# Kernel tuning notes

Hardware: AMD Instinct MI355X
Metric: run time of the kernel (lower is better)

Reference implementation:

```python
import jax, jax.numpy as jnp
import numpy as np

# bucket boundaries from the original module; bucket = last index with width >= bin
BUCKET_BINS = jnp.array([0, 1, 2, 3, 4, 5, 7, 8, 15, 16, 31, 32, 63, 64], dtype=jnp.int32)


def setup_inputs() -> dict:
    key = jax.random.key(0)
    k1, k2, k3, k4, k5 = jax.random.split(key, 5)
    B, S, D, E = 16, 512, 768, 128   # batch, n_spans, span_dim, distance_embeddings_dim
    T, O = 64, 64                    # targets / opinions per batch element
    spans = jax.random.normal(k1, (B, S, D), dtype=jnp.float32)
    dist_emb = jax.random.normal(k2, (len(BUCKET_BINS), E), dtype=jnp.float32) * 0.02
    span_indices = jnp.sort(jax.random.randint(k3, (S, 2), 0, 128, dtype=jnp.int32), axis=1)
    target_indices = jax.random.randint(k4, (B, T), 0, S, dtype=jnp.int32)
    opinion_indices = jax.random.randint(k5, (B, O), 0, S, dtype=jnp.int32)
    return {"spans": spans, "dist_emb": dist_emb, "span_indices": span_indices,
            "target_indices": target_indices, "opinion_indices": opinion_indices}


def reference(spans, dist_emb, span_indices, target_indices, opinion_indices):
    # spans: [B,S,D]; span_indices: [S,2]; target/opinion_indices: [B,T]/[B,O]
    B, T = target_indices.shape
    O = opinion_indices.shape[1]
    # itertools.product order: for each target, iterate all opinions
    pair_t = jnp.repeat(target_indices, O, axis=1)      # [B, P] with P = T*O
    pair_o = jnp.tile(opinion_indices, (1, T))          # [B, P]
    # gather span representations
    span_t = jnp.take_along_axis(spans, pair_t[:, :, None], axis=1)  # [B,P,D]
    span_o = jnp.take_along_axis(spans, pair_o[:, :, None], axis=1)  # [B,P,D]
    # gather (a,b) / (c,d) word positions and compute min distance
    ab = span_indices[pair_t]                            # [B,P,2]
    cd = span_indices[pair_o]                            # [B,P,2]
    a, b = ab[..., 0], ab[..., 1]
    c, d = cd[..., 0], cd[..., 1]
    width = jnp.minimum(jnp.abs(b - c), jnp.abs(a - d))  # [B,P]
    # bucketize: last index with width >= BUCKET_BINS[idx]
    bucket = jnp.searchsorted(BUCKET_BINS, width.astype(jnp.int32), side="right") - 1
    dist = dist_emb[bucket]                              # [B,P,E]
    # G(St, So) = [St; So; f_distance]
    out = jnp.concatenate([span_t, span_o, dist], axis=-1)  # [B,P,2D+E]
    return out
```

## Files before the change

kernel.cpp:

```cpp
#include <hip/hip_runtime.h>


#define B_DIM 16
#define S_DIM 512
#define D_DIM 768
#define E_DIM 128
#define T_DIM 64
#define O_DIM 64
#define ROW_FLOATS (2 * D_DIM + E_DIM)
#define ROW_F4 (ROW_FLOATS / 4)
#define D_F4 (D_DIM / 4)

typedef float f32x4 __attribute__((ext_vector_type(4)));

__global__ __launch_bounds__(256) void pair_rep_kernel(
    const float* __restrict__ spans,
    const float* __restrict__ dist_emb,
    const int*   __restrict__ span_indices,
    const int*   __restrict__ target_indices,
    const int*   __restrict__ opinion_indices,
    float*       __restrict__ out)
{
    const int row = blockIdx.x;
    const int b   = row >> 12;
    const int p   = row & 4095;
    const int t   = p >> 6;
    const int o   = p & 63;

    const int ti = target_indices[b * T_DIM + t];
    const int oi = opinion_indices[b * O_DIM + o];

    const int a_ = span_indices[2 * ti];
    const int b_ = span_indices[2 * ti + 1];
    const int c_ = span_indices[2 * oi];
    const int d_ = span_indices[2 * oi + 1];
    const int w1 = abs(b_ - c_);
    const int w2 = abs(a_ - d_);
    const int width = min(w1, w2);

    const int bins[14] = {0, 1, 2, 3, 4, 5, 7, 8, 15, 16, 31, 32, 63, 64};
    int bucket = -1;
#pragma unroll
    for (int i = 0; i < 14; ++i) bucket += (width >= bins[i]) ? 1 : 0;

    const f32x4* st = (const f32x4*)(spans + ((size_t)b * S_DIM + ti) * D_DIM);
    const f32x4* so = (const f32x4*)(spans + ((size_t)b * S_DIM + oi) * D_DIM);
    const f32x4* de = (const f32x4*)(dist_emb + (size_t)bucket * E_DIM);
    f32x4* dst = (f32x4*)(out + (size_t)row * ROW_FLOATS);

    for (int c4 = threadIdx.x; c4 < ROW_F4; c4 += 256) {
        f32x4 v;
        if (c4 < D_F4) {
            v = st[c4];
        } else if (c4 < 2 * D_F4) {
            v = so[c4 - D_F4];
        } else {
            v = de[c4 - 2 * D_F4];
        }
        dst[c4] = v;
    }
}

extern "C" void kernel_launch(void* const* d_in, const int* in_sizes, int n_in,
                              void* d_out, int out_size, void* d_ws, size_t ws_size,
                              hipStream_t stream) {
    const float* spans           = (const float*)d_in[0];
    const float* dist_emb        = (const float*)d_in[1];
    const int*   span_indices    = (const int*)d_in[2];
    const int*   target_indices  = (const int*)d_in[3];
    const int*   opinion_indices = (const int*)d_in[4];
    float* out = (float*)d_out;

    const int n_rows = B_DIM * T_DIM * O_DIM;
    pair_rep_kernel<<<n_rows, 256, 0, stream>>>(
        spans, dist_emb, span_indices, target_indices, opinion_indices, out);
}
```

Before: 473.9 us.

## Tile output into 8x8 target-opinion blocks and reuse loaded span rows

Replaces the one-block-per-output-row kernel with blocks covering an 8x8 tile of target/opinion pairs. Each thread loads a span vector once per target or opinion into registers and writes it to eight output rows. Separate thread groups handle the target section, the opinion section and the distance embedding. The aim is to cut redundant gather reads and per-row index and bucket work, which matters because the kernel is bound by writing about 400MB of output. The trade-off is far fewer blocks (1024 instead of 65536), each doing many strided stores, which may lower parallelism and memory-level concurrency.

```diff
diff --git a/kernel.cpp b/kernel.cpp
--- a/kernel.cpp
+++ b/kernel.cpp
@@ -8,12 +8,14 @@
 #define T_DIM 64
 #define O_DIM 64
 #define ROW_FLOATS (2 * D_DIM + E_DIM)
-#define ROW_F4 (ROW_FLOATS / 4)
 #define D_F4 (D_DIM / 4)
+#define E_F4 (E_DIM / 4)
+#define TB 8
+#define OB 8
 
 typedef float f32x4 __attribute__((ext_vector_type(4)));
 
-__global__ __launch_bounds__(256) void pair_rep_kernel(
+__global__ __launch_bounds__(448) void pair_rep_tiled(
     const float* __restrict__ spans,
     const float* __restrict__ dist_emb,
     const int*   __restrict__ span_indices,
@@ -21,43 +23,74 @@
     const int*   __restrict__ opinion_indices,
     float*       __restrict__ out)
 {
-    const int row = blockIdx.x;
-    const int b   = row >> 12;
-    const int p   = row & 4095;
-    const int t   = p >> 6;
-    const int o   = p & 63;
+    const int blk  = blockIdx.x;
+    const int b    = blk >> 6;
+    const int tile = blk & 63;
+    const int ti0  = (tile >> 3) << 3;
+    const int oj0  = (tile & 7) << 3;
+    const int tid  = threadIdx.x;
 
-    const int ti = target_indices[b * T_DIM + t];
-    const int oi = opinion_indices[b * O_DIM + o];
+    int tidx[TB], oidx[OB];
+#pragma unroll
+    for (int i = 0; i < TB; ++i) tidx[i] = target_indices[b * T_DIM + ti0 + i];
+#pragma unroll
+    for (int j = 0; j < OB; ++j) oidx[j] = opinion_indices[b * O_DIM + oj0 + j];
 
-    const int a_ = span_indices[2 * ti];
-    const int b_ = span_indices[2 * ti + 1];
-    const int c_ = span_indices[2 * oi];
-    const int d_ = span_indices[2 * oi + 1];
-    const int w1 = abs(b_ - c_);
-    const int w2 = abs(a_ - d_);
-    const int width = min(w1, w2);
+    const size_t row00 = ((size_t)b * 4096 + (size_t)ti0 * 64 + oj0) * ROW_FLOATS;
 
-    const int bins[14] = {0, 1, 2, 3, 4, 5, 7, 8, 15, 16, 31, 32, 63, 64};
-    int bucket = -1;
+    if (tid < D_F4) {
+        const int c4 = tid;
+        f32x4 r[TB];
 #pragma unroll
-    for (int i = 0; i < 14; ++i) bucket += (width >= bins[i]) ? 1 : 0;
-
-    const f32x4* st = (const f32x4*)(spans + ((size_t)b * S_DIM + ti) * D_DIM);
-    const f32x4* so = (const f32x4*)(spans + ((size_t)b * S_DIM + oi) * D_DIM);
-    const f32x4* de = (const f32x4*)(dist_emb + (size_t)bucket * E_DIM);
-    f32x4* dst = (f32x4*)(out + (size_t)row * ROW_FLOATS);
-
-    for (int c4 = threadIdx.x; c4 < ROW_F4; c4 += 256) {
-        f32x4 v;
-        if (c4 < D_F4) {
-            v = st[c4];
-        } else if (c4 < 2 * D_F4) {
-            v = so[c4 - D_F4];
-        } else {
-            v = de[c4 - 2 * D_F4];
+        for (int i = 0; i < TB; ++i)
+            r[i] = ((const f32x4*)(spans + ((size_t)b * S_DIM + tidx[i]) * D_DIM))[c4];
+#pragma unroll
+        for (int i = 0; i < TB; ++i) {
+            float* rowp = out + row00 + (size_t)i * 64 * ROW_FLOATS + (size_t)c4 * 4;
+#pragma unroll
+            for (int j = 0; j < OB; ++j)
+                *(f32x4*)(rowp + (size_t)j * ROW_FLOATS) = r[i];
         }
-        dst[c4] = v;
+    } else if (tid < 2 * D_F4) {
+        const int c4 = tid - D_F4;
+        f32x4 r[OB];
+#pragma unroll
+        for (int j = 0; j < OB; ++j)
+            r[j] = ((const f32x4*)(spans + ((size_t)b * S_DIM + oidx[j]) * D_DIM))[c4];
+#pragma unroll
+        for (int i = 0; i < TB; ++i) {
+            float* rowp = out + row00 + (size_t)i * 64 * ROW_FLOATS + D_DIM + (size_t)c4 * 4;
+#pragma unroll
+            for (int j = 0; j < OB; ++j)
+                *(f32x4*)(rowp + (size_t)j * ROW_FLOATS) = r[j];
+        }
+    } else if (tid < 2 * D_F4 + E_F4) {
+        const int c = tid - 2 * D_F4;
+        int a_[TB], b_[TB], c_[OB], d_[OB];
+#pragma unroll
+        for (int i = 0; i < TB; ++i) {
+            a_[i] = span_indices[2 * tidx[i]];
+            b_[i] = span_indices[2 * tidx[i] + 1];
+        }
+#pragma unroll
+        for (int j = 0; j < OB; ++j) {
+            c_[j] = span_indices[2 * oidx[j]];
+            d_[j] = span_indices[2 * oidx[j] + 1];
+        }
+        const int bins[14] = {0, 1, 2, 3, 4, 5, 7, 8, 15, 16, 31, 32, 63, 64};
+#pragma unroll
+        for (int i = 0; i < TB; ++i) {
+            float* rowp = out + row00 + (size_t)i * 64 * ROW_FLOATS + 2 * D_DIM + (size_t)c * 4;
+#pragma unroll
+            for (int j = 0; j < OB; ++j) {
+                const int width = min(abs(b_[i] - c_[j]), abs(a_[i] - d_[j]));
+                int bucket = -1;
+#pragma unroll
+                for (int k = 0; k < 14; ++k) bucket += (width >= bins[k]) ? 1 : 0;
+                const f32x4 v = ((const f32x4*)(dist_emb + (size_t)bucket * E_DIM))[c];
+                *(f32x4*)(rowp + (size_t)j * ROW_FLOATS) = v;
+            }
+        }
     }
 }
 
@@ -71,7 +104,7 @@
     const int*   opinion_indices = (const int*)d_in[4];
     float* out = (float*)d_out;
 
-    const int n_rows = B_DIM * T_DIM * O_DIM;
-    pair_rep_kernel<<<n_rows, 256, 0, stream>>>(
+    const int n_blocks = B_DIM * (T_DIM / TB) * (O_DIM / OB);
+    pair_rep_tiled<<<n_blocks, 448, 0, stream>>>(
         spans, dist_emb, span_indices, target_indices, opinion_indices, out);
 }
```

Result: faster. 457.7 us (-3.4%).

## Process 32 pair rows per block with wave-per-row and register-cached target

Applied to the files above, without the earlier changes.

Each block now handles 32 consecutive pair rows sharing one target; the target span row is loaded once into registers per wave and reused for every row. Each wave writes a whole row with straight-line vector stores instead of a branchy strided loop. Block indices are also swizzled across eight groups. This aims to cut per-block launch and index overhead and redundant target loads, at the cost of fewer blocks and a larger per-wave register footprint.

```diff
diff --git a/kernel.cpp b/kernel.cpp
--- a/kernel.cpp
+++ b/kernel.cpp
@@ -8,12 +8,12 @@
 #define T_DIM 64
 #define O_DIM 64
 #define ROW_FLOATS (2 * D_DIM + E_DIM)
-#define ROW_F4 (ROW_FLOATS / 4)
-#define D_F4 (D_DIM / 4)
+#define ROWS_PER_BLOCK 32
+#define N_BLOCKS (B_DIM * T_DIM * O_DIM / ROWS_PER_BLOCK)
 
 typedef float f32x4 __attribute__((ext_vector_type(4)));
 
-__global__ __launch_bounds__(256) void pair_rep_kernel(
+__global__ __launch_bounds__(256) void pair_rep_seq(
     const float* __restrict__ spans,
     const float* __restrict__ dist_emb,
     const int*   __restrict__ span_indices,
@@ -21,43 +21,53 @@
     const int*   __restrict__ opinion_indices,
     float*       __restrict__ out)
 {
-    const int row = blockIdx.x;
-    const int b   = row >> 12;
-    const int p   = row & 4095;
-    const int t   = p >> 6;
-    const int o   = p & 63;
+    const int blk0 = blockIdx.x;
+    const int blk  = (blk0 & 7) * (N_BLOCKS / 8) + (blk0 >> 3);
 
-    const int ti = target_indices[b * T_DIM + t];
-    const int oi = opinion_indices[b * O_DIM + o];
+    const int b  = blk >> 7;
+    const int r0 = (blk & 127) * ROWS_PER_BLOCK;
+    const int t  = r0 >> 6;
+    const int wave = threadIdx.x >> 6;
+    const int lane = threadIdx.x & 63;
 
-    const int a_ = span_indices[2 * ti];
-    const int b_ = span_indices[2 * ti + 1];
-    const int c_ = span_indices[2 * oi];
-    const int d_ = span_indices[2 * oi + 1];
-    const int w1 = abs(b_ - c_);
-    const int w2 = abs(a_ - d_);
-    const int width = min(w1, w2);
+    const int ti  = target_indices[b * T_DIM + t];
+    const int ab0 = span_indices[2 * ti];
+    const int ab1 = span_indices[2 * ti + 1];
+
+    const f32x4* trow = (const f32x4*)(spans + ((size_t)b * S_DIM + ti) * D_DIM);
+    const f32x4 t0 = trow[lane];
+    const f32x4 t1 = trow[64 + lane];
+    const f32x4 t2 = trow[128 + lane];
 
     const int bins[14] = {0, 1, 2, 3, 4, 5, 7, 8, 15, 16, 31, 32, 63, 64};
-    int bucket = -1;
+
+    for (int rr = wave; rr < ROWS_PER_BLOCK; rr += 4) {
+        const int r  = r0 + rr;
+        const int o  = r & 63;
+        const int oi = opinion_indices[b * O_DIM + o];
+        const int c0 = span_indices[2 * oi];
+        const int d0 = span_indices[2 * oi + 1];
+        const int width = min(abs(ab1 - c0), abs(ab0 - d0));
+        int bucket = -1;
 #pragma unroll
-    for (int i = 0; i < 14; ++i) bucket += (width >= bins[i]) ? 1 : 0;
+        for (int k = 0; k < 14; ++k) bucket += (width >= bins[k]) ? 1 : 0;
 
-    const f32x4* st = (const f32x4*)(spans + ((size_t)b * S_DIM + ti) * D_DIM);
-    const f32x4* so = (const f32x4*)(spans + ((size_t)b * S_DIM + oi) * D_DIM);
-    const f32x4* de = (const f32x4*)(dist_emb + (size_t)bucket * E_DIM);
-    f32x4* dst = (f32x4*)(out + (size_t)row * ROW_FLOATS);
+        const f32x4* orow = (const f32x4*)(spans + ((size_t)b * S_DIM + oi) * D_DIM);
+        float* dst = out + ((size_t)b * 4096 + r) * ROW_FLOATS;
 
-    for (int c4 = threadIdx.x; c4 < ROW_F4; c4 += 256) {
-        f32x4 v;
-        if (c4 < D_F4) {
-            v = st[c4];
-        } else if (c4 < 2 * D_F4) {
-            v = so[c4 - D_F4];
-        } else {
-            v = de[c4 - 2 * D_F4];
+        const f32x4 o0 = orow[lane];
+        const f32x4 o1 = orow[64 + lane];
+        const f32x4 o2 = orow[128 + lane];
+        *(f32x4*)(dst + (size_t)lane * 4)            = t0;
+        *(f32x4*)(dst + (size_t)(64 + lane) * 4)     = t1;
+        *(f32x4*)(dst + (size_t)(128 + lane) * 4)    = t2;
+        *(f32x4*)(dst + (size_t)(192 + lane) * 4)    = o0;
+        *(f32x4*)(dst + (size_t)(256 + lane) * 4)    = o1;
+        *(f32x4*)(dst + (size_t)(320 + lane) * 4)    = o2;
+        if (lane < 32) {
+            const f32x4 dv = ((const f32x4*)(dist_emb + (size_t)bucket * E_DIM))[lane];
+            *(f32x4*)(dst + (size_t)(384 + lane) * 4) = dv;
         }
-        dst[c4] = v;
     }
 }
 
@@ -71,7 +81,6 @@
     const int*   opinion_indices = (const int*)d_in[4];
     float* out = (float*)d_out;
 
-    const int n_rows = B_DIM * T_DIM * O_DIM;
-    pair_rep_kernel<<<n_rows, 256, 0, stream>>>(
+    pair_rep_seq<<<N_BLOCKS, 256, 0, stream>>>(
         spans, dist_emb, span_indices, target_indices, opinion_indices, out);
 }
```

Result: faster. 448.0 us (-5.5%).
